# Optimization experiments

Measured on AMD Instinct MI355X. Metric: run time of the kernel, lower is better.

## Reference

```python
import jax, jax.numpy as jnp
import numpy as np

BETA = 0.25


def setup_inputs() -> dict:
    key = jax.random.key(0)
    k1, k2 = jax.random.split(key)
    ze = jax.random.normal(k1, (16, 64, 64, 64), dtype=jnp.float32)  # (B, L, H, W)
    # codebook init mirrors uniform_(-1/K, 1/K)
    K = 1024
    emb = jax.random.uniform(k2, (K, 64), dtype=jnp.float32, minval=-1.0 / K, maxval=1.0 / K)
    return {"ze": ze, "emb": emb}


def reference(ze, emb):
    B, L, H, W = ze.shape
    K = emb.shape[0]
    # (B, H, W, L) -> (N, L)
    zf = jnp.transpose(ze, (0, 2, 3, 1)).reshape(-1, L)
    # squared euclidean distances (N, K)
    d = (jnp.sum(zf * zf, axis=1, keepdims=True)
         + jnp.sum(emb * emb, axis=1)
         - 2.0 * zf @ emb.T)
    idx = jnp.argmin(d, axis=1)  # (N,)
    # direct gather == one-hot @ emb
    z_q = jnp.transpose(emb[idx].reshape(B, H, W, L), (0, 3, 1, 2))
    loss = (jnp.mean((jax.lax.stop_gradient(z_q) - ze) ** 2)
            + BETA * jnp.mean((z_q - jax.lax.stop_gradient(ze)) ** 2))
    # straight-through estimator
    z_q_st = ze + jax.lax.stop_gradient(z_q - ze)
    # perplexity of code usage
    counts = jnp.zeros((K,), dtype=zf.dtype).at[idx].add(1.0)
    e_mean = counts / zf.shape[0]
    perplexity = jnp.exp(-jnp.sum(e_mean * jnp.log(e_mean + 1e-10)))
    return z_q_st, loss, idx.reshape(-1, 1)
```

## Files before the change

kernel.cpp:

```cpp
#include <hip/hip_runtime.h>

typedef short bf16x8 __attribute__((ext_vector_type(8)));
typedef float f32x4  __attribute__((ext_vector_type(4)));

#define CAP 12

#define WS_LOSS 0
#define WS_DONE 8
#define WS_EN   64
#define WS_EBF  4160

#define L_EBF    0
#define L_MARG   131072
#define L_CCNT   132096
#define L_KCH    133120
#define L_CSLOT  134144
#define L_TOTAL  146432

__device__ __forceinline__ unsigned short f2bf(float f) {
    unsigned u = __float_as_uint(f);
    return (unsigned short)((u + 0x7fffu + ((u >> 16) & 1u)) >> 16);
}

__device__ __forceinline__ float np_pairwise_sumsq64(const float* a) {
    float r[8];
    #pragma unroll
    for (int j = 0; j < 8; ++j) r[j] = __fmul_rn(a[j], a[j]);
    #pragma unroll
    for (int i = 8; i < 64; i += 8)
        #pragma unroll
        for (int j = 0; j < 8; ++j)
            r[j] = __fadd_rn(r[j], __fmul_rn(a[i + j], a[i + j]));
    return __fadd_rn(
        __fadd_rn(__fadd_rn(r[0], r[1]), __fadd_rn(r[2], r[3])),
        __fadd_rn(__fadd_rn(r[4], r[5]), __fadd_rn(r[6], r[7])));
}

__global__ __launch_bounds__(256) void prep_kernel(
    const float* __restrict__ emb, unsigned short* __restrict__ ebf,
    float* __restrict__ en_t,
    float* __restrict__ loss, int* __restrict__ done)
{
    int k = blockIdx.x * 256 + threadIdx.x;
    if (k == 0) { *loss = 0.0f; *done = 0; }
    if (k < 1024) {
        float e[64];
        #pragma unroll
        for (int l = 0; l < 64; ++l) e[l] = emb[k * 64 + l];
        en_t[k] = np_pairwise_sumsq64(e);
        int tile = k >> 4, r = k & 15;
        #pragma unroll
        for (int j = 0; j < 8; ++j) {
            bf16x8 v;
            #pragma unroll
            for (int m = 0; m < 8; ++m) v[m] = (short)f2bf(e[j * 8 + m]);
            *(bf16x8*)(ebf + tile * 1024 + j * 128 + r * 8) = v;
        }
    }
}

__global__ __launch_bounds__(512, 2)
void vq_kernel(
    const float* __restrict__ ze, const float* __restrict__ emb,
    const unsigned short* __restrict__ ebf, const float* __restrict__ en_t,
    float* __restrict__ out_zq, float* __restrict__ out_idxf,
    float* __restrict__ loss, int* __restrict__ done,
    float* __restrict__ out_loss)
{
    extern __shared__ char smem[];
    unsigned short* ebf_l = (unsigned short*)(smem + L_EBF);
    float*          marg_l= (float*)(smem + L_MARG);
    int*            ccnt  = (int*)(smem + L_CCNT);
    int*            kch   = (int*)(smem + L_KCH);
    int*            cslot = (int*)(smem + L_CSLOT);

    const int t = threadIdx.x;
    const int n0 = blockIdx.x * 256;
    const int gbase = (n0 >> 12) * 262144 + (n0 & 4095);

    {
        const bf16x8* src = (const bf16x8*)ebf;
        bf16x8* dst = (bf16x8*)ebf_l;
        #pragma unroll 16
        for (int i = 0; i < 16; ++i) dst[t + i * 512] = src[t + i * 512];
    }

    const int wv = t >> 6, lane = t & 63;
    const int r = lane & 15, q = lane >> 4;
    const int wp = wv * 32;
    bf16x8 a[2][2];
    float sm[2] = {0.f, 0.f};
    #pragma unroll
    for (int rg = 0; rg < 2; ++rg) {
        const float* zb = ze + gbase + wp + rg * 16 + r;
        #pragma unroll
        for (int j = 0; j < 8; ++j) {
            const float v0 = zb[(q * 8 + j) * 4096];
            const float v1 = zb[(32 + q * 8 + j) * 4096];
            a[rg][0][j] = (short)f2bf(v0);
            a[rg][1][j] = (short)f2bf(v1);
            sm[rg] += fabsf(v0) + fabsf(v1);
        }
    }
    #pragma unroll
    for (int rg = 0; rg < 2; ++rg) {
        float s = sm[rg];
        s += __shfl_xor(s, 16, 64);
        s += __shfl_xor(s, 32, 64);
        if (q == 0) marg_l[wp + rg * 16 + r] = 1.67e-5f * s + 2.0e-4f;
    }
    if (t < 256) ccnt[t] = 0;
    __syncthreads();

    const unsigned short* bptr = ebf_l + q * 128 + r * 8;

    float rm[8];
    #pragma unroll
    for (int i = 0; i < 8; ++i) rm[i] = -1e30f;
    {
        bf16x8 pb0[4], pb1[4];
        #pragma unroll
        for (int i = 0; i < 4; ++i) {
            pb0[i] = *(const bf16x8*)(bptr + i * 1024);
            pb1[i] = *(const bf16x8*)(bptr + i * 1024 + 512);
        }
        #pragma unroll 4
        for (int tile = 0; tile < 64; ++tile) {
            bf16x8 b0 = pb0[tile & 3], b1 = pb1[tile & 3];
            int nt = tile + 4; if (nt > 63) nt = 63;
            pb0[tile & 3] = *(const bf16x8*)(bptr + nt * 1024);
            pb1[tile & 3] = *(const bf16x8*)(bptr + nt * 1024 + 512);
            #pragma unroll
            for (int rg = 0; rg < 2; ++rg) {
                f32x4 c = {0.f, 0.f, 0.f, 0.f};
                c = __builtin_amdgcn_mfma_f32_16x16x32_bf16(a[rg][0], b0, c, 0, 0, 0);
                c = __builtin_amdgcn_mfma_f32_16x16x32_bf16(a[rg][1], b1, c, 0, 0, 0);
                #pragma unroll
                for (int i = 0; i < 4; ++i)
                    rm[rg * 4 + i] = fmaxf(rm[rg * 4 + i], c[i]);
            }
        }
    }
    #pragma unroll
    for (int j = 0; j < 8; ++j) {
        float v = rm[j];
        v = fmaxf(v, __shfl_xor(v, 1, 16));
        v = fmaxf(v, __shfl_xor(v, 2, 16));
        v = fmaxf(v, __shfl_xor(v, 4, 16));
        v = fmaxf(v, __shfl_xor(v, 8, 16));
        rm[j] = v;
    }
    float thr[8];
    #pragma unroll
    for (int j = 0; j < 8; ++j) {
        const int row = wp + (j >> 2) * 16 + q * 4 + (j & 3);
        thr[j] = rm[j] - 0.5f * marg_l[row];
    }

    {
        bf16x8 pb0[4], pb1[4];
        #pragma unroll
        for (int i = 0; i < 4; ++i) {
            pb0[i] = *(const bf16x8*)(bptr + i * 1024);
            pb1[i] = *(const bf16x8*)(bptr + i * 1024 + 512);
        }
        #pragma unroll 4
        for (int tile = 0; tile < 64; ++tile) {
            bf16x8 b0 = pb0[tile & 3], b1 = pb1[tile & 3];
            int nt = tile + 4; if (nt > 63) nt = 63;
            pb0[tile & 3] = *(const bf16x8*)(bptr + nt * 1024);
            pb1[tile & 3] = *(const bf16x8*)(bptr + nt * 1024 + 512);
            const int code = tile * 16 + r;
            #pragma unroll
            for (int rg = 0; rg < 2; ++rg) {
                f32x4 c = {0.f, 0.f, 0.f, 0.f};
                c = __builtin_amdgcn_mfma_f32_16x16x32_bf16(a[rg][0], b0, c, 0, 0, 0);
                c = __builtin_amdgcn_mfma_f32_16x16x32_bf16(a[rg][1], b1, c, 0, 0, 0);
                #pragma unroll
                for (int i = 0; i < 4; ++i) {
                    if (c[i] >= thr[rg * 4 + i]) {
                        const int pp = wp + rg * 16 + q * 4 + i;
                        const int ci = atomicAdd(&ccnt[pp], 1);
                        if (ci < CAP) cslot[pp * CAP + ci] = code;
                    }
                }
            }
        }
    }
    __syncthreads();

    {
        const int p = t >> 1, cl = t & 1;
        int cnt = ccnt[p]; if (cnt > CAP) cnt = CAP;
        float z[64];
        const float* zp = ze + gbase + p;
        #pragma unroll
        for (int l = 0; l < 64; ++l) z[l] = zp[l * 4096];
        const float znorm = np_pairwise_sumsq64(z);
        float best = 1e30f; int bk = 1 << 20;
        for (int c = cl; c < cnt; c += 2) {
            const int k = cslot[p * CAP + c];
            const float4* er = (const float4*)(emb + k * 64);
            float acc = 0.0f;
            #pragma unroll
            for (int jj = 0; jj < 16; ++jj) {
                const float4 v = er[jj];
                acc = fmaf(z[4 * jj + 0], v.x, acc);
                acc = fmaf(z[4 * jj + 1], v.y, acc);
                acc = fmaf(z[4 * jj + 2], v.z, acc);
                acc = fmaf(z[4 * jj + 3], v.w, acc);
            }
            const float sc = __fsub_rn(__fadd_rn(znorm, en_t[k]), __fmul_rn(2.0f, acc));
            if (sc < best || (sc == best && k < bk)) { best = sc; bk = k; }
        }
        const float ob = __shfl_xor(best, 1, 64);
        const int   ok = __shfl_xor(bk, 1, 64);
        if (ob < best || (ob == best && ok < bk)) { best = ob; bk = ok; }
        if (cl == 0) {
            kch[p] = bk;
            out_idxf[n0 + p] = (float)bk;
        }
    }
    __syncthreads();

    {
        const int p = t & 255, h = t >> 8;
        const int bk = kch[p];
        const float* er = emb + bk * 64 + h * 32;
        const float* zp = ze + gbase + p + (h * 32) * 4096;
        float* op = out_zq + gbase + p + (h * 32) * 4096;
        float ls = 0.0f;
        #pragma unroll
        for (int j = 0; j < 32; ++j) {
            const float qv = er[j];
            const float zv = zp[j * 4096];
            op[j * 4096] = qv;
            const float d = qv - zv;
            ls = fmaf(d, d, ls);
        }
        #pragma unroll
        for (int off = 32; off > 0; off >>= 1) ls += __shfl_down(ls, off, 64);
        if (lane == 0) atomicAdd(loss, ls);
    }

    __syncthreads();
    if (t == 0) {
        __threadfence();
        int old = atomicAdd(done, 1);
        if (old == (int)gridDim.x - 1) {
            __threadfence();
            float total = atomicAdd(loss, 0.0f);
            *out_loss = 1.25f * total / 4194304.0f;
        }
    }
}

extern "C" void kernel_launch(void* const* d_in, const int* in_sizes, int n_in,
                              void* d_out, int out_size, void* d_ws, size_t ws_size,
                              hipStream_t stream)
{
    const float* ze  = (const float*)d_in[0];
    const float* emb = (const float*)d_in[1];
    float* out = (float*)d_out;
    float* out_zq   = out;
    float* out_loss = out + 4194304;
    float* out_idxf = out + 4194305;

    char* w = (char*)d_ws;
    float*          ws_loss = (float*)(w + WS_LOSS);
    int*            ws_done = (int*)(w + WS_DONE);
    float*          ws_en   = (float*)(w + WS_EN);
    unsigned short* ebf     = (unsigned short*)(w + WS_EBF);

    static bool attr_set = false;
    if (!attr_set) {
        hipFuncSetAttribute((const void*)vq_kernel,
                            hipFuncAttributeMaxDynamicSharedMemorySize, L_TOTAL);
        attr_set = true;
    }

    prep_kernel<<<4, 256, 0, stream>>>(emb, ebf, ws_en, ws_loss, ws_done);
    vq_kernel<<<256, 512, L_TOTAL, stream>>>(ze, emb, ebf, ws_en, out_zq,
                                             out_idxf, ws_loss, ws_done, out_loss);
}
```

Before: 140.0 us.

## Split codebook across waves with 128-row A tiles staged through LDS

```diff
diff --git a/kernel.cpp b/kernel.cpp
--- a/kernel.cpp
+++ b/kernel.cpp
@@ -11,11 +11,14 @@
 #define WS_EBF  4160
 
 #define L_EBF    0
-#define L_MARG   131072
-#define L_CCNT   132096
-#define L_KCH    133120
-#define L_CSLOT  134144
-#define L_TOTAL  146432
+#define L_X      131072
+#define L_THR    131072
+#define L_CSLOT  132096
+#define L_RM4    147456
+#define L_CCNT   151552
+#define L_KCH    152576
+#define L_MPART  153600
+#define L_TOTAL  155648
 
 __device__ __forceinline__ unsigned short f2bf(float f) {
     unsigned u = __float_as_uint(f);
@@ -69,14 +72,22 @@
 {
     extern __shared__ char smem[];
     unsigned short* ebf_l = (unsigned short*)(smem + L_EBF);
-    float*          marg_l= (float*)(smem + L_MARG);
+    unsigned short* zbf   = (unsigned short*)(smem + L_X);
+    float*          thr_l = (float*)(smem + L_THR);
+    int*            cslot = (int*)(smem + L_CSLOT);
+    float*          rm4   = (float*)(smem + L_RM4);
     int*            ccnt  = (int*)(smem + L_CCNT);
     int*            kch   = (int*)(smem + L_KCH);
-    int*            cslot = (int*)(smem + L_CSLOT);
+    float*          mpart = (float*)(smem + L_MPART);
 
     const int t = threadIdx.x;
     const int n0 = blockIdx.x * 256;
     const int gbase = (n0 >> 12) * 262144 + (n0 & 4095);
+
+    const int wv = t >> 6, lane = t & 63;
+    const int r = lane & 15, q = lane >> 4;
+    const int pg = wv & 1, kf = wv >> 1;
+    const int wp = pg * 128;
 
     {
         const bf16x8* src = (const bf16x8*)ebf;
@@ -85,53 +96,98 @@
         for (int i = 0; i < 16; ++i) dst[t + i * 512] = src[t + i * 512];
     }
 
-    const int wv = t >> 6, lane = t & 63;
-    const int r = lane & 15, q = lane >> 4;
-    const int wp = wv * 32;
-    bf16x8 a[2][2];
-    float sm[2] = {0.f, 0.f};
+    {
+        const int p = t & 127, dc = t >> 7;
+        const float* zp = ze + gbase + p;
+        unsigned short us[16];
+        float s = 0.0f;
+        #pragma unroll
+        for (int j = 0; j < 16; ++j) {
+            const float v = zp[(dc * 16 + j) * 4096];
+            us[j] = f2bf(v);
+            s += fabsf(v);
+        }
+        const int sw = (p & 7) << 3;
+        unsigned short* row = zbf + p * 64;
+        *(bf16x8*)(row + ((dc * 16 + 0) ^ sw)) = *(bf16x8*)(us);
+        *(bf16x8*)(row + ((dc * 16 + 8) ^ sw)) = *(bf16x8*)(us + 8);
+        mpart[p * 4 + dc] = s;
+    }
+    __syncthreads();
+
+    bf16x8 a[8][2];
+    float marg_reg = 0.0f;
+
+    if (pg == 0) {
+        const int sw = (r & 7) << 3;
+        #pragma unroll
+        for (int rg = 0; rg < 8; ++rg) {
+            const unsigned short* row = zbf + (rg * 16 + r) * 64;
+            a[rg][0] = *(const bf16x8*)(row + ((q * 8) ^ sw));
+            a[rg][1] = *(const bf16x8*)(row + ((32 + q * 8) ^ sw));
+        }
+    }
+    if (t < 128) {
+        const float S = mpart[t * 4 + 0] + mpart[t * 4 + 1]
+                      + mpart[t * 4 + 2] + mpart[t * 4 + 3];
+        marg_reg = 1.67e-5f * S + 2.0e-4f;
+    }
+    __syncthreads();
+
+    {
+        const int p = t & 127, dc = t >> 7;
+        const float* zp = ze + gbase + 128 + p;
+        unsigned short us[16];
+        float s = 0.0f;
+        #pragma unroll
+        for (int j = 0; j < 16; ++j) {
+            const float v = zp[(dc * 16 + j) * 4096];
+            us[j] = f2bf(v);
+            s += fabsf(v);
+        }
+        const int sw = (p & 7) << 3;
+        unsigned short* row = zbf + p * 64;
+        *(bf16x8*)(row + ((dc * 16 + 0) ^ sw)) = *(bf16x8*)(us);
+        *(bf16x8*)(row + ((dc * 16 + 8) ^ sw)) = *(bf16x8*)(us + 8);
+        mpart[p * 4 + dc] = s;
+    }
+    __syncthreads();
+
+    if (pg == 1) {
+        const int sw = (r & 7) << 3;
+        #pragma unroll
+        for (int rg = 0; rg < 8; ++rg) {
+            const unsigned short* row = zbf + (rg * 16 + r) * 64;
+            a[rg][0] = *(const bf16x8*)(row + ((q * 8) ^ sw));
+            a[rg][1] = *(const bf16x8*)(row + ((32 + q * 8) ^ sw));
+        }
+    }
+    if (t >= 128 && t < 256) {
+        const int p = t - 128;
+        const float S = mpart[p * 4 + 0] + mpart[p * 4 + 1]
+                      + mpart[p * 4 + 2] + mpart[p * 4 + 3];
+        marg_reg = 1.67e-5f * S + 2.0e-4f;
+    }
+
+    const unsigned short* bptr = ebf_l + (kf * 16) * 1024 + q * 128 + r * 8;
+
+    float rm[32];
     #pragma unroll
-    for (int rg = 0; rg < 2; ++rg) {
-        const float* zb = ze + gbase + wp + rg * 16 + r;
-        #pragma unroll
-        for (int j = 0; j < 8; ++j) {
-            const float v0 = zb[(q * 8 + j) * 4096];
-            const float v1 = zb[(32 + q * 8 + j) * 4096];
-            a[rg][0][j] = (short)f2bf(v0);
-            a[rg][1][j] = (short)f2bf(v1);
-            sm[rg] += fabsf(v0) + fabsf(v1);
-        }
-    }
-    #pragma unroll
-    for (int rg = 0; rg < 2; ++rg) {
-        float s = sm[rg];
-        s += __shfl_xor(s, 16, 64);
-        s += __shfl_xor(s, 32, 64);
-        if (q == 0) marg_l[wp + rg * 16 + r] = 1.67e-5f * s + 2.0e-4f;
-    }
-    if (t < 256) ccnt[t] = 0;
-    __syncthreads();
-
-    const unsigned short* bptr = ebf_l + q * 128 + r * 8;
-
-    float rm[8];
-    #pragma unroll
-    for (int i = 0; i < 8; ++i) rm[i] = -1e30f;
-    {
-        bf16x8 pb0[4], pb1[4];
-        #pragma unroll
-        for (int i = 0; i < 4; ++i) {
-            pb0[i] = *(const bf16x8*)(bptr + i * 1024);
-            pb1[i] = *(const bf16x8*)(bptr + i * 1024 + 512);
-        }
+    for (int i = 0; i < 32; ++i) rm[i] = -1e30f;
+    {
+        bf16x8 pb0[2], pb1[2];
+        pb0[0] = *(const bf16x8*)(bptr);
+        pb1[0] = *(const bf16x8*)(bptr + 512);
+        pb0[1] = *(const bf16x8*)(bptr + 1024);
+        pb1[1] = *(const bf16x8*)(bptr + 1536);
         #pragma unroll 4
-        for (int tile = 0; tile < 64; ++tile) {
-            bf16x8 b0 = pb0[tile & 3], b1 = pb1[tile & 3];
-            int nt = tile + 4; if (nt > 63) nt = 63;
-            pb0[tile & 3] = *(const bf16x8*)(bptr + nt * 1024);
-            pb1[tile & 3] = *(const bf16x8*)(bptr + nt * 1024 + 512);
+        for (int tile = 0; tile < 16; ++tile) {
+            bf16x8 b0 = pb0[tile & 1], b1 = pb1[tile & 1];
+            int nt = tile + 2; if (nt > 15) nt = 15;
+            pb0[tile & 1] = *(const bf16x8*)(bptr + nt * 1024);
+            pb1[tile & 1] = *(const bf16x8*)(bptr + nt * 1024 + 512);
             #pragma unroll
-            for (int rg = 0; rg < 2; ++rg) {
+            for (int rg = 0; rg < 8; ++rg) {
                 f32x4 c = {0.f, 0.f, 0.f, 0.f};
                 c = __builtin_amdgcn_mfma_f32_16x16x32_bf16(a[rg][0], b0, c, 0, 0, 0);
                 c = __builtin_amdgcn_mfma_f32_16x16x32_bf16(a[rg][1], b1, c, 0, 0, 0);
@@ -142,37 +198,44 @@
         }
     }
     #pragma unroll
-    for (int j = 0; j < 8; ++j) {
+    for (int j = 0; j < 32; ++j) {
         float v = rm[j];
         v = fmaxf(v, __shfl_xor(v, 1, 16));
         v = fmaxf(v, __shfl_xor(v, 2, 16));
         v = fmaxf(v, __shfl_xor(v, 4, 16));
         v = fmaxf(v, __shfl_xor(v, 8, 16));
-        rm[j] = v;
-    }
-    float thr[8];
-    #pragma unroll
-    for (int j = 0; j < 8; ++j) {
-        const int row = wp + (j >> 2) * 16 + q * 4 + (j & 3);
-        thr[j] = rm[j] - 0.5f * marg_l[row];
-    }
-
-    {
-        bf16x8 pb0[4], pb1[4];
-        #pragma unroll
-        for (int i = 0; i < 4; ++i) {
-            pb0[i] = *(const bf16x8*)(bptr + i * 1024);
-            pb1[i] = *(const bf16x8*)(bptr + i * 1024 + 512);
-        }
+        if (r == 0)
+            rm4[(wp + (j >> 2) * 16 + q * 4 + (j & 3)) * 4 + kf] = v;
+    }
+    __syncthreads();
+
+    if (t < 256) {
+        const float maxc = fmaxf(fmaxf(rm4[t * 4 + 0], rm4[t * 4 + 1]),
+                                 fmaxf(rm4[t * 4 + 2], rm4[t * 4 + 3]));
+        thr_l[t] = maxc - 0.5f * marg_reg;
+        ccnt[t] = 0;
+    }
+    __syncthreads();
+
+    {
+        float thr[32];
+        #pragma unroll
+        for (int j = 0; j < 32; ++j)
+            thr[j] = thr_l[wp + (j >> 2) * 16 + q * 4 + (j & 3)];
+        bf16x8 pb0[2], pb1[2];
+        pb0[0] = *(const bf16x8*)(bptr);
+        pb1[0] = *(const bf16x8*)(bptr + 512);
+        pb0[1] = *(const bf16x8*)(bptr + 1024);
+        pb1[1] = *(const bf16x8*)(bptr + 1536);
         #pragma unroll 4
-        for (int tile = 0; tile < 64; ++tile) {
-            bf16x8 b0 = pb0[tile & 3], b1 = pb1[tile & 3];
-            int nt = tile + 4; if (nt > 63) nt = 63;
-            pb0[tile & 3] = *(const bf16x8*)(bptr + nt * 1024);
-            pb1[tile & 3] = *(const bf16x8*)(bptr + nt * 1024 + 512);
-            const int code = tile * 16 + r;
+        for (int tile = 0; tile < 16; ++tile) {
+            bf16x8 b0 = pb0[tile & 1], b1 = pb1[tile & 1];
+            int nt = tile + 2; if (nt > 15) nt = 15;
+            pb0[tile & 1] = *(const bf16x8*)(bptr + nt * 1024);
+            pb1[tile & 1] = *(const bf16x8*)(bptr + nt * 1024 + 512);
+            const int code = kf * 256 + tile * 16 + r;
             #pragma unroll
-            for (int rg = 0; rg < 2; ++rg) {
+            for (int rg = 0; rg < 8; ++rg) {
                 f32x4 c = {0.f, 0.f, 0.f, 0.f};
                 c = __builtin_amdgcn_mfma_f32_16x16x32_bf16(a[rg][0], b0, c, 0, 0, 0);
                 c = __builtin_amdgcn_mfma_f32_16x16x32_bf16(a[rg][1], b1, c, 0, 0, 0);
```

Measured after the change: 140.7 us. About the same (+0.5%).

## Double threads per block so each wave handles sixteen rows instead of thirty-two

Applied to the files above, without the earlier changes.

```diff
diff --git a/kernel.cpp b/kernel.cpp
--- a/kernel.cpp
+++ b/kernel.cpp
@@ -59,7 +59,7 @@
     }
 }
 
-__global__ __launch_bounds__(512, 2)
+__global__ __launch_bounds__(1024, 4)
 void vq_kernel(
     const float* __restrict__ ze, const float* __restrict__ emb,
     const unsigned short* __restrict__ ebf, const float* __restrict__ en_t,
@@ -81,42 +81,40 @@
     {
         const bf16x8* src = (const bf16x8*)ebf;
         bf16x8* dst = (bf16x8*)ebf_l;
-        #pragma unroll 16
-        for (int i = 0; i < 16; ++i) dst[t + i * 512] = src[t + i * 512];
+        #pragma unroll 8
+        for (int i = 0; i < 8; ++i) dst[t + i * 1024] = src[t + i * 1024];
     }
 
     const int wv = t >> 6, lane = t & 63;
     const int r = lane & 15, q = lane >> 4;
-    const int wp = wv * 32;
-    bf16x8 a[2][2];
-    float sm[2] = {0.f, 0.f};
-    #pragma unroll
-    for (int rg = 0; rg < 2; ++rg) {
-        const float* zb = ze + gbase + wp + rg * 16 + r;
+    const int wp = wv * 16;
+    bf16x8 a0, a1;
+    float sm = 0.0f;
+    {
+        const float* zb = ze + gbase + wp + r;
         #pragma unroll
         for (int j = 0; j < 8; ++j) {
             const float v0 = zb[(q * 8 + j) * 4096];
             const float v1 = zb[(32 + q * 8 + j) * 4096];
-            a[rg][0][j] = (short)f2bf(v0);
-            a[rg][1][j] = (short)f2bf(v1);
-            sm[rg] += fabsf(v0) + fabsf(v1);
-        }
-    }
-    #pragma unroll
-    for (int rg = 0; rg < 2; ++rg) {
-        float s = sm[rg];
+            a0[j] = (short)f2bf(v0);
+            a1[j] = (short)f2bf(v1);
+            sm += fabsf(v0) + fabsf(v1);
+        }
+    }
+    {
+        float s = sm;
         s += __shfl_xor(s, 16, 64);
         s += __shfl_xor(s, 32, 64);
-        if (q == 0) marg_l[wp + rg * 16 + r] = 1.67e-5f * s + 2.0e-4f;
+        if (q == 0) marg_l[wp + r] = 1.67e-5f * s + 2.0e-4f;
     }
     if (t < 256) ccnt[t] = 0;
     __syncthreads();
 
     const unsigned short* bptr = ebf_l + q * 128 + r * 8;
 
-    float rm[8];
-    #pragma unroll
-    for (int i = 0; i < 8; ++i) rm[i] = -1e30f;
+    float rm[4];
+    #pragma unroll
+    for (int i = 0; i < 4; ++i) rm[i] = -1e30f;
     {
         bf16x8 pb0[4], pb1[4];
         #pragma unroll
@@ -130,19 +128,16 @@
             int nt = tile + 4; if (nt > 63) nt = 63;
             pb0[tile & 3] = *(const bf16x8*)(bptr + nt * 1024);
             pb1[tile & 3] = *(const bf16x8*)(bptr + nt * 1024 + 512);
-            #pragma unroll
-            for (int rg = 0; rg < 2; ++rg) {
-                f32x4 c = {0.f, 0.f, 0.f, 0.f};
-                c = __builtin_amdgcn_mfma_f32_16x16x32_bf16(a[rg][0], b0, c, 0, 0, 0);
-                c = __builtin_amdgcn_mfma_f32_16x16x32_bf16(a[rg][1], b1, c, 0, 0, 0);
-                #pragma unroll
-                for (int i = 0; i < 4; ++i)
-                    rm[rg * 4 + i] = fmaxf(rm[rg * 4 + i], c[i]);
-            }
-        }
-    }
-    #pragma unroll
-    for (int j = 0; j < 8; ++j) {
+            f32x4 c = {0.f, 0.f, 0.f, 0.f};
+            c = __builtin_amdgcn_mfma_f32_16x16x32_bf16(a0, b0, c, 0, 0, 0);
+            c = __builtin_amdgcn_mfma_f32_16x16x32_bf16(a1, b1, c, 0, 0, 0);
+            #pragma unroll
+            for (int i = 0; i < 4; ++i)
+                rm[i] = fmaxf(rm[i], c[i]);
+        }
+    }
+    #pragma unroll
+    for (int j = 0; j < 4; ++j) {
         float v = rm[j];
         v = fmaxf(v, __shfl_xor(v, 1, 16));
         v = fmaxf(v, __shfl_xor(v, 2, 16));
@@ -150,12 +145,10 @@
         v = fmaxf(v, __shfl_xor(v, 8, 16));
         rm[j] = v;
     }
-    float thr[8];
-    #pragma unroll
-    for (int j = 0; j < 8; ++j) {
-        const int row = wp + (j >> 2) * 16 + q * 4 + (j & 3);
-        thr[j] = rm[j] - 0.5f * marg_l[row];
-    }
+    float thr[4];
+    #pragma unroll
+    for (int j = 0; j < 4; ++j)
+        thr[j] = rm[j] - 0.5f * marg_l[wp + q * 4 + j];
 
     {
         bf16x8 pb0[4], pb1[4];
@@ -171,18 +164,15 @@
             pb0[tile & 3] = *(const bf16x8*)(bptr + nt * 1024);
             pb1[tile & 3] = *(const bf16x8*)(bptr + nt * 1024 + 512);
             const int code = tile * 16 + r;
-            #pragma unroll
-            for (int rg = 0; rg < 2; ++rg) {
-                f32x4 c = {0.f, 0.f, 0.f, 0.f};
-                c = __builtin_amdgcn_mfma_f32_16x16x32_bf16(a[rg][0], b0, c, 0, 0, 0);
-                c = __builtin_amdgcn_mfma_f32_16x16x32_bf16(a[rg][1], b1, c, 0, 0, 0);
-                #pragma unroll
-                for (int i = 0; i < 4; ++i) {
-                    if (c[i] >= thr[rg * 4 + i]) {
-                        const int pp = wp + rg * 16 + q * 4 + i;
-                        const int ci = atomicAdd(&ccnt[pp], 1);
-                        if (ci < CAP) cslot[pp * CAP + ci] = code;
-                    }
+            f32x4 c = {0.f, 0.f, 0.f, 0.f};
+            c = __builtin_amdgcn_mfma_f32_16x16x32_bf16(a0, b0, c, 0, 0, 0);
+            c = __builtin_amdgcn_mfma_f32_16x16x32_bf16(a1, b1, c, 0, 0, 0);
+            #pragma unroll
+            for (int i = 0; i < 4; ++i) {
+                if (c[i] >= thr[i]) {
+                    const int pp = wp + q * 4 + i;
+                    const int ci = atomicAdd(&ccnt[pp], 1);
+                    if (ci < CAP) cslot[pp * CAP + ci] = code;
                 }
             }
         }
@@ -190,7 +180,7 @@
     __syncthreads();
 
     {
-        const int p = t >> 1, cl = t & 1;
+        const int p = t >> 2, cl = t & 3;
         int cnt = ccnt[p]; if (cnt > CAP) cnt = CAP;
         float z[64];
         const float* zp = ze + gbase + p;
@@ -198,7 +188,7 @@
         for (int l = 0; l < 64; ++l) z[l] = zp[l * 4096];
         const float znorm = np_pairwise_sumsq64(z);
         float best = 1e30f; int bk = 1 << 20;
-        for (int c = cl; c < cnt; c += 2) {
+        for (int c = cl; c < cnt; c += 4) {
             const int k = cslot[p * CAP + c];
             const float4* er = (const float4*)(emb + k * 64);
             float acc = 0.0f;
@@ -213,9 +203,12 @@
             const float sc = __fsub_rn(__fadd_rn(znorm, en_t[k]), __fmul_rn(2.0f, acc));
             if (sc < best || (sc == best && k < bk)) { best = sc; bk = k; }
         }
-        const float ob = __shfl_xor(best, 1, 64);
-        const int   ok = __shfl_xor(bk, 1, 64);
-        if (ob < best || (ob == best && ok < bk)) { best = ob; bk = ok; }
+        #pragma unroll
+        for (int m = 1; m < 4; m <<= 1) {
+            const float ob = __shfl_xor(best, m, 4);
+            const int   ok = __shfl_xor(bk, m, 4);
+            if (ob < best || (ob == best && ok < bk)) { best = ob; bk = ok; }
+        }
         if (cl == 0) {
             kch[p] = bk;
             out_idxf[n0 + p] = (float)bk;
@@ -226,16 +219,19 @@
     {
         const int p = t & 255, h = t >> 8;
         const int bk = kch[p];
-        const float* er = emb + bk * 64 + h * 32;
-        const float* zp = ze + gbase + p + (h * 32) * 4096;
-        float* op = out_zq + gbase + p + (h * 32) * 4096;
+        const float* er = emb + bk * 64 + h * 16;
+        const float* zp = ze + gbase + p + (h * 16) * 4096;
+        float* op = out_zq + gbase + p + (h * 16) * 4096;
+        float ev[16], zv[16];
+        #pragma unroll
+        for (int j = 0; j < 16; ++j) ev[j] = er[j];
+        #pragma unroll
+        for (int j = 0; j < 16; ++j) zv[j] = zp[j * 4096];
         float ls = 0.0f;
         #pragma unroll
-        for (int j = 0; j < 32; ++j) {
-            const float qv = er[j];
-            const float zv = zp[j * 4096];
-            op[j * 4096] = qv;
-            const float d = qv - zv;
+        for (int j = 0; j < 16; ++j) {
+            op[j * 4096] = ev[j];
+            const float d = ev[j] - zv[j];
             ls = fmaf(d, d, ls);
         }
         #pragma unroll
@@ -280,6 +276,6 @@
     }
 
     prep_kernel<<<4, 256, 0, stream>>>(emb, ebf, ws_en, ws_loss, ws_done);
-    vq_kernel<<<256, 512, L_TOTAL, stream>>>(ze, emb, ebf, ws_en, out_zq,
-                                             out_idxf, ws_loss, ws_done, out_loss);
-}
+    vq_kernel<<<256, 1024, L_TOTAL, stream>>>(ze, emb, ebf, ws_en, out_zq,
+                                              out_idxf, ws_loss, ws_done, out_loss);
+}
```

Result: slower. 155.4 us (+11.0%).
